# Kernel optimization log

Hardware: AMD Instinct MI355X
Metric: run time of the kernel (lower is better)

Reference implementation:

```python
import jax, jax.numpy as jnp
import numpy as np

N_NODES = 100000
N_EDGES = 3200000
N_GRAPHS = 512
IN_CH = 50
HID = 256


def setup_inputs() -> dict:
    key = jax.random.key(0)
    ks = jax.random.split(key, 8)
    x = jax.random.normal(ks[0], (N_NODES, IN_CH), dtype=jnp.float32)
    edge_index = jax.random.randint(ks[1], (2, N_EDGES), 0, N_NODES, dtype=jnp.int64)
    batch = jnp.sort(jax.random.randint(ks[2], (N_NODES,), 0, N_GRAPHS, dtype=jnp.int64))
    # SAGEConv params: lin_l (applied to aggregated neighbors, with bias), lin_r (root, no bias)
    s_in = 1.0 / np.sqrt(IN_CH)
    W_l = jax.random.uniform(ks[3], (HID, IN_CH), jnp.float32, -s_in, s_in)
    b_l = jax.random.uniform(ks[4], (HID,), jnp.float32, -s_in, s_in)
    W_r = jax.random.uniform(ks[5], (HID, IN_CH), jnp.float32, -s_in, s_in)
    s_h = 1.0 / np.sqrt(HID)
    W_c = jax.random.uniform(ks[6], (2, HID), jnp.float32, -s_h, s_h)
    b_c = jax.random.uniform(ks[7], (2,), jnp.float32, -s_h, s_h)
    return {"x": x, "edge_index": edge_index, "batch": batch,
            "W_l": W_l, "b_l": b_l, "W_r": W_r, "W_c": W_c, "b_c": b_c}


def _segment_mean(vals, seg_ids, num_segments):
    s = jax.ops.segment_sum(vals, seg_ids, num_segments=num_segments)
    cnt = jax.ops.segment_sum(jnp.ones((vals.shape[0],), vals.dtype), seg_ids,
                              num_segments=num_segments)
    return s / jnp.maximum(cnt, 1.0)[:, None]


def reference(x, edge_index, batch, W_l, b_l, W_r, W_c, b_c):
    src, dst = edge_index[0], edge_index[1]
    # SAGEConv: mean-aggregate neighbor features at each target node
    agg = _segment_mean(x[src], dst, N_NODES)          # [N, IN_CH]
    h = agg @ W_l.T + b_l + x @ W_r.T                  # [N, HID]
    h = jax.nn.leaky_relu(h, negative_slope=0.01)
    # dropout p=0.3 is identity in eval mode
    pooled = _segment_mean(h, batch, N_GRAPHS)         # [G, HID]
    return pooled @ W_c.T + b_c                        # [G, 2]
```

## Files before the change

### kernel.cpp

```cpp
#include <hip/hip_runtime.h>

#define N_NODES 100000
#define N_EDGES 3200000
#define N_GRAPHS 512
#define IN_CH 50
#define HID 256
#define NB 391
#define NBLK2 391
#define EPB2 8192

typedef unsigned short ushort_t;
using s16x8 = __attribute__((ext_vector_type(8))) short;
using us8   = __attribute__((ext_vector_type(8))) unsigned short;
using us4   = __attribute__((ext_vector_type(4))) unsigned short;
using f32x4 = __attribute__((ext_vector_type(4))) float;
using f32x2 = __attribute__((ext_vector_type(2))) float;

__device__ __forceinline__ float bf2f(ushort_t u) {
    return __uint_as_float(((unsigned int)u) << 16);
}
__device__ __forceinline__ ushort_t f2bf(float f) {
    unsigned int x = __float_as_uint(f);
    unsigned int r = x + 0x7fffu + ((x >> 16) & 1u);
    return (ushort_t)(r >> 16);
}
__device__ __forceinline__ int clampi(int v, int hi) {
    return v < 0 ? 0 : (v >= hi ? hi - 1 : v);
}

__device__ __forceinline__ unsigned char f2e4(float f) {
    unsigned char s = (unsigned char)((__float_as_uint(f) >> 31) << 7);
    float a = fabsf(f);
    if (a >= 0.015625f) {
        if (a > 448.f) a = 448.f;
        unsigned int u = __float_as_uint(a);
        u += 0x7FFFFu + ((u >> 20) & 1u);
        int e8 = (int)(u >> 23) - 127 + 7;
        unsigned int m8 = (u >> 20) & 7u;
        if (e8 > 15) { e8 = 15; m8 = 6; }
        return s | (unsigned char)((e8 << 3) | m8);
    } else {
        int m = (int)rintf(a * 512.f);
        if (m > 7) return s | 0x08;
        return s | (unsigned char)m;
    }
}
__device__ __forceinline__ float e42f(unsigned int c) {
    unsigned int w = ((c & 0x80u) << 24) | ((c & 0x7fu) << 20);
    return __uint_as_float(w) * 0x1p120f;
}

__device__ __forceinline__ void acc8(f32x2 a2[4], uint2 w, float m) {
#if __has_builtin(__builtin_amdgcn_cvt_pk_f32_fp8)
    f32x2 p0 = __builtin_amdgcn_cvt_pk_f32_fp8((int)w.x, false);
    f32x2 p1 = __builtin_amdgcn_cvt_pk_f32_fp8((int)w.x, true);
    f32x2 p2 = __builtin_amdgcn_cvt_pk_f32_fp8((int)w.y, false);
    f32x2 p3 = __builtin_amdgcn_cvt_pk_f32_fp8((int)w.y, true);
#else
    f32x2 p0, p1, p2, p3;
    p0[0] = e42f(w.x & 0xffu);         p0[1] = e42f((w.x >> 8) & 0xffu);
    p1[0] = e42f((w.x >> 16) & 0xffu); p1[1] = e42f((w.x >> 24) & 0xffu);
    p2[0] = e42f(w.y & 0xffu);         p2[1] = e42f((w.y >> 8) & 0xffu);
    p3[0] = e42f((w.y >> 16) & 0xffu); p3[1] = e42f((w.y >> 24) & 0xffu);
#endif
    a2[0] = p0 * m + a2[0];
    a2[1] = p1 * m + a2[1];
    a2[2] = p2 * m + a2[2];
    a2[3] = p3 * m + a2[3];
}

__device__ __forceinline__ void wavered(f32x2 a2[4]) {
#pragma unroll
    for (int p = 0; p < 4; ++p) {
        a2[p][0] += __shfl_xor(a2[p][0], 8);
        a2[p][1] += __shfl_xor(a2[p][1], 8);
        a2[p][0] += __shfl_xor(a2[p][0], 16);
        a2[p][1] += __shfl_xor(a2[p][1], 16);
        a2[p][0] += __shfl_xor(a2[p][0], 32);
        a2[p][1] += __shfl_xor(a2[p][1], 32);
    }
}

constexpr size_t OFF_GACC   = 0;
constexpr size_t ZBYTES     = 8192;
constexpr size_t OFF_AGG    = 561536;
constexpr size_t OFF_X8     = 13361536;
constexpr size_t OFF_EP     = 19761536;
constexpr size_t OFF_WT     = 32573824;
constexpr size_t OFF_BND    = 32639360;
constexpr size_t OFF_LST    = 32641416;

__global__ __launch_bounds__(512) void k_scatter(const int* __restrict__ ei,
                                                 int* __restrict__ ep,
                                                 ushort_t* __restrict__ lst) {
    __shared__ int hist[NB];
    __shared__ int sa[512];
    __shared__ int sorig[512];
    __shared__ int lstart[NB + 1];
    __shared__ int lcur[NB];
    __shared__ unsigned int eph[EPB2];

    const int blk = blockIdx.x, t = threadIdx.x;
    for (int i = t; i < NB; i += 512) hist[i] = 0;
    __syncthreads();
    const int e0 = blk * EPB2;
    int sv[16], dv[16];
#pragma unroll
    for (int j = 0; j < 16; ++j) {
        int e = e0 + j * 512 + t;
        if (e < N_EDGES) {
            sv[j] = clampi(ei[e], N_NODES);
            dv[j] = clampi(ei[N_EDGES + e], N_NODES);
        } else {
            dv[j] = -1;
        }
    }
#pragma unroll
    for (int j = 0; j < 16; ++j)
        if (dv[j] >= 0) atomicAdd(&hist[dv[j] >> 8], 1);
    __syncthreads();
    int v = (t < NB) ? hist[t] : 0;
    sa[t] = v; sorig[t] = v;
    __syncthreads();
    for (int off = 1; off < 512; off <<= 1) {
        int u = (t >= off) ? sa[t - off] : 0;
        __syncthreads();
        sa[t] += u;
        __syncthreads();
    }
    if (t < NB) { lstart[t] = sa[t] - sorig[t]; lcur[t] = sa[t] - sorig[t]; }
    if (t == NB - 1) lstart[NB] = sa[t];
    __syncthreads();
#pragma unroll
    for (int j = 0; j < 16; ++j) {
        if (dv[j] >= 0) {
            int b = dv[j] >> 8;
            int r = atomicAdd(&lcur[b], 1);
            eph[r] = ((unsigned int)sv[j] << 8) | (unsigned int)(dv[j] & 255);
        }
    }
    __syncthreads();
    int mv = lstart[NB];
    for (int i = t; i < mv; i += 512) ep[e0 + i] = (int)eph[i];
    for (int i = t; i <= NB; i += 512) lst[blk * (NB + 1) + i] = (ushort_t)lstart[i];
}

#define PREP_CONV_BLOCKS 6250
#define PREP_BW_BLOCKS 128
#define PREP_BND_BLOCKS 391
__global__ __launch_bounds__(256) void k_prep(const float* __restrict__ x,
                                              unsigned char* __restrict__ x8,
                                              const float* __restrict__ Wl,
                                              const float* __restrict__ Wr,
                                              ushort_t* __restrict__ WT,
                                              const int* __restrict__ batch,
                                              int* __restrict__ bnd) {
    int blk = blockIdx.x;
    if (blk < PREP_CONV_BLOCKS) {
        int idx = blk * 256 + threadIdx.x;
        int n = idx >> 4, c4 = (idx & 15) << 2;
        uchar4 o;
        o.x = (c4 + 0 < IN_CH) ? f2e4(x[n * IN_CH + c4 + 0]) : (unsigned char)0;
        o.y = (c4 + 1 < IN_CH) ? f2e4(x[n * IN_CH + c4 + 1]) : (unsigned char)0;
        o.z = (c4 + 2 < IN_CH) ? f2e4(x[n * IN_CH + c4 + 2]) : (unsigned char)0;
        o.w = (c4 + 3 < IN_CH) ? f2e4(x[n * IN_CH + c4 + 3]) : (unsigned char)0;
        *(uchar4*)(x8 + (size_t)n * 64 + c4) = o;
    } else if (blk < PREP_CONV_BLOCKS + PREP_BW_BLOCKS) {
        int idx = (blk - PREP_CONV_BLOCKS) * 256 + threadIdx.x;
        int j = idx >> 7;
        int k = idx & 127;
        ushort_t val = 0;
        if (k < IN_CH) val = f2bf(Wl[j * IN_CH + k]);
        else if (k >= 64 && k < 64 + IN_CH) val = f2bf(Wr[j * IN_CH + (k - 64)]);
        WT[idx] = val;
    } else {
        int n = (blk - PREP_CONV_BLOCKS - PREP_BW_BLOCKS) * 256 + threadIdx.x;
        if (n >= N_NODES) return;
        int b = clampi(batch[n], N_GRAPHS);
        if (n == 0) {
            for (int g = 0; g <= b; ++g) bnd[g] = 0;
        } else {
            int a = clampi(batch[n - 1], N_GRAPHS);
            for (int g = a + 1; g <= b; ++g) bnd[g] = n;
        }
        if (n == N_NODES - 1) {
            for (int g = b + 1; g <= N_GRAPHS; ++g) bnd[g] = N_NODES;
        }
    }
}

#define CSR_CAP 10240
__global__ __launch_bounds__(512) void k_csrgather(const int* __restrict__ ep,
                                                   const ushort_t* __restrict__ lst,
                                                   const unsigned char* __restrict__ x8,
                                                   ushort_t* __restrict__ agg) {
    __shared__ int sa[512];
    __shared__ int sorig[512];
    __shared__ int rro[NBLK2 + 1];
    __shared__ int lsa[NBLK2];
    __shared__ int ldeg[256];
    __shared__ int lcur[256];
    __shared__ int excl_s[256];
    __shared__ int lds_src[CSR_CAP];
    ushort_t* runof = (ushort_t*)lds_src;

    const int b = blockIdx.x, t = threadIdx.x;

    int lenv = 0;
    if (t < NBLK2) {
        int lsv = (int)lst[t * (NB + 1) + b];
        int le = (int)lst[t * (NB + 1) + b + 1];
        lenv = le - lsv;
        lsa[t] = lsv;
    }
    sa[t] = lenv; sorig[t] = lenv;
    __syncthreads();
    for (int off = 1; off < 512; off <<= 1) {
        int u = (t >= off) ? sa[t - off] : 0;
        __syncthreads();
        sa[t] += u;
        __syncthreads();
    }
    if (t < NBLK2) rro[t] = sa[t] - sorig[t];
    if (t == NBLK2 - 1) rro[NBLK2] = sa[t];
    __syncthreads();
    int m = rro[NBLK2];
    if (m > CSR_CAP) m = CSR_CAP;

    if (t < NBLK2) {
        int o = rro[t];
        int e = o + lenv;
        if (e > CSR_CAP) e = CSR_CAP;
        for (int j = o; j < e; ++j) runof[j] = (ushort_t)t;
    }
    if (t < 256) ldeg[t] = 0;
    __syncthreads();

    int rv[20];
#pragma unroll
    for (int k = 0; k < 20; ++k) {
        int i = t + k * 512;
        if (i < m) {
            int r = (int)runof[i];
            rv[k] = ep[r * EPB2 + lsa[r] + (i - rro[r])];
        }
    }
#pragma unroll
    for (int k = 0; k < 20; ++k) {
        int i = t + k * 512;
        if (i < m) atomicAdd(&ldeg[rv[k] & 255], 1);
    }
    __syncthreads();
    if (t < 256) sa[t] = ldeg[t];
    __syncthreads();
    for (int off = 1; off < 256; off <<= 1) {
        int u = (t >= off && t < 256) ? sa[t - off] : 0;
        __syncthreads();
        if (t < 256) sa[t] += u;
        __syncthreads();
    }
    if (t < 256) {
        int excl = sa[t] - ldeg[t];
        excl_s[t] = excl;
        lcur[t] = excl;
    }
    __syncthreads();
#pragma unroll
    for (int k = 0; k < 20; ++k) {
        int i = t + k * 512;
        if (i < m) {
            int p = rv[k];
            int r = atomicAdd(&lcur[p & 255], 1);
            lds_src[r] = p >> 8;
        }
    }
    __syncthreads();

    const int wv = t >> 6;
    const int lane = t & 63;
    const int r8 = lane >> 3;
    const int c8 = lane & 7;
    const int cb = c8 << 3;
    for (int k = 0; k < 32; k += 2) {
        int ln0 = wv * 32 + k;
        int gid0 = (b << 8) + ln0;
        if (gid0 >= N_NODES) break;
        int ok1 = (gid0 + 1 < N_NODES) ? 1 : 0;
        int dg0 = ldeg[ln0], st0 = excl_s[ln0];
        int dg1 = ok1 ? ldeg[ln0 + 1] : 0;
        int st1 = ok1 ? excl_s[ln0 + 1] : st0;

        f32x2 a2[4] = {};
        f32x2 c2[4] = {};
        int dgm = dg0 > dg1 ? dg0 : dg1;
        int nit = (dgm + 31) >> 5;
        for (int it = 0; it < nit; ++it) {
            int i0 = (it << 5) + r8;
            int i1 = i0 + 8, i2 = i0 + 16, i3 = i0 + 24;
            int sA = lds_src[st0 + (i0 < dg0 ? i0 : 0)];
            int sB = lds_src[st0 + (i1 < dg0 ? i1 : 0)];
            int sC = lds_src[st0 + (i2 < dg0 ? i2 : 0)];
            int sD = lds_src[st0 + (i3 < dg0 ? i3 : 0)];
            int sE = lds_src[st1 + (i0 < dg1 ? i0 : 0)];
            int sF = lds_src[st1 + (i1 < dg1 ? i1 : 0)];
            int sG = lds_src[st1 + (i2 < dg1 ? i2 : 0)];
            int sH = lds_src[st1 + (i3 < dg1 ? i3 : 0)];
            uint2 wA = *(const uint2*)(x8 + (size_t)sA * 64 + cb);
            uint2 wB = *(const uint2*)(x8 + (size_t)sB * 64 + cb);
            uint2 wC = *(const uint2*)(x8 + (size_t)sC * 64 + cb);
            uint2 wD = *(const uint2*)(x8 + (size_t)sD * 64 + cb);
            uint2 wE = *(const uint2*)(x8 + (size_t)sE * 64 + cb);
            uint2 wF = *(const uint2*)(x8 + (size_t)sF * 64 + cb);
            uint2 wG = *(const uint2*)(x8 + (size_t)sG * 64 + cb);
            uint2 wH = *(const uint2*)(x8 + (size_t)sH * 64 + cb);
            acc8(a2, wA, i0 < dg0 ? 1.f : 0.f);
            acc8(a2, wB, i1 < dg0 ? 1.f : 0.f);
            acc8(a2, wC, i2 < dg0 ? 1.f : 0.f);
            acc8(a2, wD, i3 < dg0 ? 1.f : 0.f);
            acc8(c2, wE, i0 < dg1 ? 1.f : 0.f);
            acc8(c2, wF, i1 < dg1 ? 1.f : 0.f);
            acc8(c2, wG, i2 < dg1 ? 1.f : 0.f);
            acc8(c2, wH, i3 < dg1 ? 1.f : 0.f);
        }
        wavered(a2);
        wavered(c2);
        if (r8 == 0) {
            float inv0 = 1.0f / (float)(dg0 > 1 ? dg0 : 1);
            us8 o;
#pragma unroll
            for (int q = 0; q < 8; ++q) o[q] = f2bf(a2[q >> 1][q & 1] * inv0);
            *(us8*)(agg + (size_t)gid0 * 64 + cb) = o;
            if (ok1) {
                float inv1 = 1.0f / (float)(dg1 > 1 ? dg1 : 1);
                us8 o1;
#pragma unroll
                for (int q = 0; q < 8; ++q) o1[q] = f2bf(c2[q >> 1][q & 1] * inv1);
                *(us8*)(agg + (size_t)(gid0 + 1) * 64 + cb) = o1;
            }
        }
    }
}

__global__ __launch_bounds__(256) void k_convb(const float* __restrict__ x,
                                               ushort_t* __restrict__ xb) {
    int t = blockIdx.x * blockDim.x + threadIdx.x;
    if (t >= N_NODES * 16) return;
    int n = t >> 4, c4 = (t & 15) << 2;
    us4 o;
#pragma unroll
    for (int j = 0; j < 4; j++) {
        int c = c4 + j;
        o[j] = (c < IN_CH) ? f2bf(x[n * IN_CH + c]) : (ushort_t)0;
    }
    *(us4*)(xb + (size_t)n * 64 + c4) = o;
}

__global__ __launch_bounds__(256) void k_gemm(const ushort_t* __restrict__ agg,
                                              const ushort_t* __restrict__ xb,
                                              const ushort_t* __restrict__ WT,
                                              const float* __restrict__ bl,
                                              const float* __restrict__ Wc,
                                              const int* __restrict__ batch,
                                              float* __restrict__ gacc) {
    __shared__ ushort_t Alds[64 * 136];
    __shared__ f32x2 yp[4][64][17];
    __shared__ float gred[64][2];

    const int t = threadIdx.x;
    const int w = t >> 6;
    const int lane = t & 63;
    const int quad = lane >> 4;
    const int r16 = lane & 15;
    const int brow0 = blockIdx.x * 128;

    if (t < 128) gred[t >> 1][t & 1] = 0.f;

    s16x8 bfr[4][4];
#pragma unroll
    for (int s = 0; s < 4; ++s)
#pragma unroll
        for (int ni = 0; ni < 4; ++ni)
            bfr[s][ni] = *(const s16x8*)(WT + (size_t)(w * 64 + 16 * ni + r16) * 128
                                            + s * 32 + (quad << 3));

    float blv[4], w0v[4], w1v[4];
#pragma unroll
    for (int ni = 0; ni < 4; ni++) {
        int col = w * 64 + 16 * ni + r16;
        blv[ni] = bl[col];
        w0v[ni] = Wc[col];
        w1v[ni] = Wc[HID + col];
    }

    int lastb = brow0 + 127;
    if (lastb >= N_NODES) lastb = N_NODES - 1;
    const int gmin = clampi(batch[brow0], N_GRAPHS);
    const int gmax = clampi(batch[lastb], N_GRAPHS);
    const int gspan = gmax - gmin + 1;
    const bool use_lds = (gspan <= 64);

    for (int r4 = 0; r4 < 2; ++r4) {
        const int row0 = brow0 + r4 * 64;
        __syncthreads();
        {
            int row = t >> 2;
            int q4 = t & 3;
            int gr = row0 + row;
            us8* dst = (us8*)&Alds[row * 136 + q4 * 32];
            if (gr < N_NODES) {
                const us8* src = (q4 < 2)
                    ? (const us8*)(agg + (size_t)gr * 64 + (q4 & 1) * 32)
                    : (const us8*)(xb + (size_t)gr * 64 + (q4 & 1) * 32);
                dst[0] = src[0];
                dst[1] = src[1];
                dst[2] = src[2];
                dst[3] = src[3];
            } else {
                us8 z = {0, 0, 0, 0, 0, 0, 0, 0};
                dst[0] = z; dst[1] = z; dst[2] = z; dst[3] = z;
            }
        }
        __syncthreads();

        f32x4 acc[4][4] = {};
#pragma unroll
        for (int s = 0; s < 4; ++s) {
            s16x8 af[4];
#pragma unroll
            for (int mi = 0; mi < 4; mi++)
                af[mi] = *(const s16x8*)&Alds[(16 * mi + r16) * 136 + s * 32 + (quad << 3)];
#pragma unroll
            for (int mi = 0; mi < 4; mi++)
#pragma unroll
                for (int ni = 0; ni < 4; ni++)
                    acc[mi][ni] = __builtin_amdgcn_mfma_f32_16x16x32_bf16(
                        af[mi], bfr[s][ni], acc[mi][ni], 0, 0, 0);
        }

#pragma unroll
        for (int mi = 0; mi < 4; mi++) {
#pragma unroll
            for (int r = 0; r < 4; r++) {
                float p0 = 0.f, p1 = 0.f;
#pragma unroll
                for (int ni = 0; ni < 4; ni++) {
                    float h = acc[mi][ni][r] + blv[ni];
                    h = (h > 0.f) ? h : 0.01f * h;
                    p0 = fmaf(h, w0v[ni], p0);
                    p1 = fmaf(h, w1v[ni], p1);
                }
                int rl = 16 * mi + (quad << 2) + r;
                f32x2 pv; pv[0] = p0; pv[1] = p1;
                yp[w][rl][r16] = pv;
            }
        }
        __syncthreads();

        if (t < 64) {
            f32x2 s; s[0] = 0.f; s[1] = 0.f;
#pragma unroll
            for (int ww = 0; ww < 4; ++ww)
#pragma unroll
                for (int j = 0; j < 16; ++j)
                    s = s + yp[ww][t][j];
            int node = row0 + t;
            if (node < N_NODES) {
                int g = clampi(batch[node], N_GRAPHS);
                if (use_lds) {
                    atomicAdd(&gred[g - gmin][0], s[0]);
                    atomicAdd(&gred[g - gmin][1], s[1]);
                } else {
                    atomicAdd(&gacc[g * 2 + 0], s[0]);
                    atomicAdd(&gacc[g * 2 + 1], s[1]);
                }
            }
        }
    }
    __syncthreads();
    if (use_lds && t < gspan * 2) {
        int gg = t >> 1, c2 = t & 1;
        float v = gred[gg][c2];
        if (v != 0.f) atomicAdd(&gacc[(gmin + gg) * 2 + c2], v);
    }
}

__global__ void k_fin(const float* __restrict__ gacc, const int* __restrict__ bnd,
                      const float* __restrict__ bc, float* __restrict__ out) {
    int t = blockIdx.x * blockDim.x + threadIdx.x;
    if (t < N_GRAPHS * 2) {
        int g = t >> 1, c = t & 1;
        int cnt = bnd[g + 1] - bnd[g];
        out[t] = gacc[t] / (float)(cnt > 1 ? cnt : 1) + bc[c];
    }
}

extern "C" void kernel_launch(void* const* d_in, const int* in_sizes, int n_in,
                              void* d_out, int out_size, void* d_ws, size_t ws_size,
                              hipStream_t stream) {
    const float* x  = (const float*)d_in[0];
    const int* ei   = (const int*)d_in[1];
    const int* batch= (const int*)d_in[2];
    const float* Wl = (const float*)d_in[3];
    const float* bl = (const float*)d_in[4];
    const float* Wr = (const float*)d_in[5];
    const float* Wc = (const float*)d_in[6];
    const float* bc = (const float*)d_in[7];
    float* out = (float*)d_out;

    char* ws = (char*)d_ws;
    float* gacc        = (float*)(ws + OFF_GACC);
    ushort_t* agg      = (ushort_t*)(ws + OFF_AGG);
    unsigned char* x8  = (unsigned char*)(ws + OFF_X8);
    int* ep            = (int*)(ws + OFF_EP);
    ushort_t* xb       = (ushort_t*)(ws + OFF_EP);
    ushort_t* WT       = (ushort_t*)(ws + OFF_WT);
    int* bnd           = (int*)(ws + OFF_BND);
    ushort_t* lst      = (ushort_t*)(ws + OFF_LST);

    hipMemsetAsync(ws, 0, ZBYTES, stream);
    k_scatter    <<<NBLK2, 512, 0, stream>>>(ei, ep, lst);
    k_prep       <<<PREP_CONV_BLOCKS + PREP_BW_BLOCKS + PREP_BND_BLOCKS, 256, 0, stream>>>(
                     x, x8, Wl, Wr, WT, batch, bnd);
    k_csrgather  <<<NB, 512, 0, stream>>>(ep, lst, x8, agg);
    k_convb      <<<(N_NODES * 16 + 255) / 256, 256, 0, stream>>>(x, xb);
    k_gemm       <<<(N_NODES + 127) / 128, 256, 0, stream>>>(agg, xb, WT, bl, Wc, batch, gacc);
    k_fin        <<<4, 256, 0, stream>>>(gacc, bnd, bc, out);
}
```

Baseline: 209.3 us.

## Fuse scatter and prep kernels; gather four nodes per wave iteration

```diff
diff --git a/kernel.cpp b/kernel.cpp
--- a/kernel.cpp
+++ b/kernel.cpp
@@ -90,9 +90,20 @@
 constexpr size_t OFF_BND    = 32639360;
 constexpr size_t OFF_LST    = 32641416;
 
-__global__ __launch_bounds__(512) void k_scatter(const int* __restrict__ ei,
-                                                 int* __restrict__ ep,
-                                                 ushort_t* __restrict__ lst) {
+#define SP_SCAT 391
+#define SP_CONV 3125
+#define SP_BW   64
+#define SP_BND  196
+__global__ __launch_bounds__(512) void k_sp(const int* __restrict__ ei,
+                                            int* __restrict__ ep,
+                                            ushort_t* __restrict__ lst,
+                                            const float* __restrict__ x,
+                                            unsigned char* __restrict__ x8,
+                                            const float* __restrict__ Wl,
+                                            const float* __restrict__ Wr,
+                                            ushort_t* __restrict__ WT,
+                                            const int* __restrict__ batch,
+                                            int* __restrict__ bnd) {
     __shared__ int hist[NB];
     __shared__ int sa[512];
     __shared__ int sorig[512];
@@ -101,63 +112,51 @@
     __shared__ unsigned int eph[EPB2];
 
     const int blk = blockIdx.x, t = threadIdx.x;
-    for (int i = t; i < NB; i += 512) hist[i] = 0;
-    __syncthreads();
-    const int e0 = blk * EPB2;
-    int sv[16], dv[16];
-#pragma unroll
-    for (int j = 0; j < 16; ++j) {
-        int e = e0 + j * 512 + t;
-        if (e < N_EDGES) {
-            sv[j] = clampi(ei[e], N_NODES);
-            dv[j] = clampi(ei[N_EDGES + e], N_NODES);
-        } else {
-            dv[j] = -1;
-        }
-    }
-#pragma unroll
-    for (int j = 0; j < 16; ++j)
-        if (dv[j] >= 0) atomicAdd(&hist[dv[j] >> 8], 1);
-    __syncthreads();
-    int v = (t < NB) ? hist[t] : 0;
-    sa[t] = v; sorig[t] = v;
-    __syncthreads();
-    for (int off = 1; off < 512; off <<= 1) {
-        int u = (t >= off) ? sa[t - off] : 0;
-        __syncthreads();
-        sa[t] += u;
-        __syncthreads();
-    }
-    if (t < NB) { lstart[t] = sa[t] - sorig[t]; lcur[t] = sa[t] - sorig[t]; }
-    if (t == NB - 1) lstart[NB] = sa[t];
-    __syncthreads();
-#pragma unroll
-    for (int j = 0; j < 16; ++j) {
-        if (dv[j] >= 0) {
-            int b = dv[j] >> 8;
-            int r = atomicAdd(&lcur[b], 1);
-            eph[r] = ((unsigned int)sv[j] << 8) | (unsigned int)(dv[j] & 255);
-        }
-    }
-    __syncthreads();
-    int mv = lstart[NB];
-    for (int i = t; i < mv; i += 512) ep[e0 + i] = (int)eph[i];
-    for (int i = t; i <= NB; i += 512) lst[blk * (NB + 1) + i] = (ushort_t)lstart[i];
-}
-
-#define PREP_CONV_BLOCKS 6250
-#define PREP_BW_BLOCKS 128
-#define PREP_BND_BLOCKS 391
-__global__ __launch_bounds__(256) void k_prep(const float* __restrict__ x,
-                                              unsigned char* __restrict__ x8,
-                                              const float* __restrict__ Wl,
-                                              const float* __restrict__ Wr,
-                                              ushort_t* __restrict__ WT,
-                                              const int* __restrict__ batch,
-                                              int* __restrict__ bnd) {
-    int blk = blockIdx.x;
-    if (blk < PREP_CONV_BLOCKS) {
-        int idx = blk * 256 + threadIdx.x;
+    if (blk < SP_SCAT) {
+        for (int i = t; i < NB; i += 512) hist[i] = 0;
+        __syncthreads();
+        const int e0 = blk * EPB2;
+        int sv[16], dv[16];
+#pragma unroll
+        for (int j = 0; j < 16; ++j) {
+            int e = e0 + j * 512 + t;
+            if (e < N_EDGES) {
+                sv[j] = clampi(ei[e], N_NODES);
+                dv[j] = clampi(ei[N_EDGES + e], N_NODES);
+            } else {
+                dv[j] = -1;
+            }
+        }
+#pragma unroll
+        for (int j = 0; j < 16; ++j)
+            if (dv[j] >= 0) atomicAdd(&hist[dv[j] >> 8], 1);
+        __syncthreads();
+        int v = (t < NB) ? hist[t] : 0;
+        sa[t] = v; sorig[t] = v;
+        __syncthreads();
+        for (int off = 1; off < 512; off <<= 1) {
+            int u = (t >= off) ? sa[t - off] : 0;
+            __syncthreads();
+            sa[t] += u;
+            __syncthreads();
+        }
+        if (t < NB) { lstart[t] = sa[t] - sorig[t]; lcur[t] = sa[t] - sorig[t]; }
+        if (t == NB - 1) lstart[NB] = sa[t];
+        __syncthreads();
+#pragma unroll
+        for (int j = 0; j < 16; ++j) {
+            if (dv[j] >= 0) {
+                int b = dv[j] >> 8;
+                int r = atomicAdd(&lcur[b], 1);
+                eph[r] = ((unsigned int)sv[j] << 8) | (unsigned int)(dv[j] & 255);
+            }
+        }
+        __syncthreads();
+        int mv = lstart[NB];
+        for (int i = t; i < mv; i += 512) ep[e0 + i] = (int)eph[i];
+        for (int i = t; i <= NB; i += 512) lst[blk * (NB + 1) + i] = (ushort_t)lstart[i];
+    } else if (blk < SP_SCAT + SP_CONV) {
+        int idx = (blk - SP_SCAT) * 512 + t;
         int n = idx >> 4, c4 = (idx & 15) << 2;
         uchar4 o;
         o.x = (c4 + 0 < IN_CH) ? f2e4(x[n * IN_CH + c4 + 0]) : (unsigned char)0;
@@ -165,8 +164,8 @@
         o.z = (c4 + 2 < IN_CH) ? f2e4(x[n * IN_CH + c4 + 2]) : (unsigned char)0;
         o.w = (c4 + 3 < IN_CH) ? f2e4(x[n * IN_CH + c4 + 3]) : (unsigned char)0;
         *(uchar4*)(x8 + (size_t)n * 64 + c4) = o;
-    } else if (blk < PREP_CONV_BLOCKS + PREP_BW_BLOCKS) {
-        int idx = (blk - PREP_CONV_BLOCKS) * 256 + threadIdx.x;
+    } else if (blk < SP_SCAT + SP_CONV + SP_BW) {
+        int idx = (blk - SP_SCAT - SP_CONV) * 512 + t;
         int j = idx >> 7;
         int k = idx & 127;
         ushort_t val = 0;
@@ -174,7 +173,7 @@
         else if (k >= 64 && k < 64 + IN_CH) val = f2bf(Wr[j * IN_CH + (k - 64)]);
         WT[idx] = val;
     } else {
-        int n = (blk - PREP_CONV_BLOCKS - PREP_BW_BLOCKS) * 256 + threadIdx.x;
+        int n = (blk - SP_SCAT - SP_CONV - SP_BW) * 512 + t;
         if (n >= N_NODES) return;
         int b = clampi(batch[n], N_GRAPHS);
         if (n == 0) {
@@ -281,61 +280,60 @@
     const int r8 = lane >> 3;
     const int c8 = lane & 7;
     const int cb = c8 << 3;
-    for (int k = 0; k < 32; k += 2) {
-        int ln0 = wv * 32 + k;
-        int gid0 = (b << 8) + ln0;
-        if (gid0 >= N_NODES) break;
-        int ok1 = (gid0 + 1 < N_NODES) ? 1 : 0;
-        int dg0 = ldeg[ln0], st0 = excl_s[ln0];
-        int dg1 = ok1 ? ldeg[ln0 + 1] : 0;
-        int st1 = ok1 ? excl_s[ln0 + 1] : st0;
-
-        f32x2 a2[4] = {};
-        f32x2 c2[4] = {};
-        int dgm = dg0 > dg1 ? dg0 : dg1;
+    for (int k = 0; k < 32; k += 4) {
+        int ln = wv * 32 + k;
+        int gid = (b << 8) + ln;
+        if (gid >= N_NODES) break;
+        int dg[4], st[4];
+#pragma unroll
+        for (int j = 0; j < 4; ++j) {
+            bool ok = (gid + j) < N_NODES;
+            dg[j] = ok ? ldeg[ln + j] : 0;
+            st[j] = ok ? excl_s[ln + j] : excl_s[ln];
+        }
+        f32x2 ac[4][4];
+#pragma unroll
+        for (int j = 0; j < 4; ++j)
+#pragma unroll
+            for (int p = 0; p < 4; ++p) { ac[j][p][0] = 0.f; ac[j][p][1] = 0.f; }
+        int dgm = dg[0];
+#pragma unroll
+        for (int j = 1; j < 4; ++j) dgm = dg[j] > dgm ? dg[j] : dgm;
         int nit = (dgm + 31) >> 5;
         for (int it = 0; it < nit; ++it) {
-            int i0 = (it << 5) + r8;
-            int i1 = i0 + 8, i2 = i0 + 16, i3 = i0 + 24;
-            int sA = lds_src[st0 + (i0 < dg0 ? i0 : 0)];
-            int sB = lds_src[st0 + (i1 < dg0 ? i1 : 0)];
-            int sC = lds_src[st0 + (i2 < dg0 ? i2 : 0)];
-            int sD = lds_src[st0 + (i3 < dg0 ? i3 : 0)];
-            int sE = lds_src[st1 + (i0 < dg1 ? i0 : 0)];
-            int sF = lds_src[st1 + (i1 < dg1 ? i1 : 0)];
-            int sG = lds_src[st1 + (i2 < dg1 ? i2 : 0)];
-            int sH = lds_src[st1 + (i3 < dg1 ? i3 : 0)];
-            uint2 wA = *(const uint2*)(x8 + (size_t)sA * 64 + cb);
-            uint2 wB = *(const uint2*)(x8 + (size_t)sB * 64 + cb);
-            uint2 wC = *(const uint2*)(x8 + (size_t)sC * 64 + cb);
-            uint2 wD = *(const uint2*)(x8 + (size_t)sD * 64 + cb);
-            uint2 wE = *(const uint2*)(x8 + (size_t)sE * 64 + cb);
-            uint2 wF = *(const uint2*)(x8 + (size_t)sF * 64 + cb);
-            uint2 wG = *(const uint2*)(x8 + (size_t)sG * 64 + cb);
-            uint2 wH = *(const uint2*)(x8 + (size_t)sH * 64 + cb);
-            acc8(a2, wA, i0 < dg0 ? 1.f : 0.f);
-            acc8(a2, wB, i1 < dg0 ? 1.f : 0.f);
-            acc8(a2, wC, i2 < dg0 ? 1.f : 0.f);
-            acc8(a2, wD, i3 < dg0 ? 1.f : 0.f);
-            acc8(c2, wE, i0 < dg1 ? 1.f : 0.f);
-            acc8(c2, wF, i1 < dg1 ? 1.f : 0.f);
-            acc8(c2, wG, i2 < dg1 ? 1.f : 0.f);
-            acc8(c2, wH, i3 < dg1 ? 1.f : 0.f);
-        }
-        wavered(a2);
-        wavered(c2);
+            int bi = (it << 5) + r8;
+            int idx[4][4];
+#pragma unroll
+            for (int j = 0; j < 4; ++j)
+#pragma unroll
+                for (int q = 0; q < 4; ++q) {
+                    int i = bi + q * 8;
+                    idx[j][q] = lds_src[st[j] + (i < dg[j] ? i : 0)];
+                }
+            uint2 wd[4][4];
+#pragma unroll
+            for (int j = 0; j < 4; ++j)
+#pragma unroll
+                for (int q = 0; q < 4; ++q)
+                    wd[j][q] = *(const uint2*)(x8 + (size_t)idx[j][q] * 64 + cb);
+#pragma unroll
+            for (int j = 0; j < 4; ++j)
+#pragma unroll
+                for (int q = 0; q < 4; ++q)
+                    acc8(ac[j], wd[j][q], (bi + q * 8) < dg[j] ? 1.f : 0.f);
+        }
+#pragma unroll
+        for (int j = 0; j < 4; ++j) wavered(ac[j]);
         if (r8 == 0) {
-            float inv0 = 1.0f / (float)(dg0 > 1 ? dg0 : 1);
-            us8 o;
-#pragma unroll
-            for (int q = 0; q < 8; ++q) o[q] = f2bf(a2[q >> 1][q & 1] * inv0);
-            *(us8*)(agg + (size_t)gid0 * 64 + cb) = o;
-            if (ok1) {
-                float inv1 = 1.0f / (float)(dg1 > 1 ? dg1 : 1);
-                us8 o1;
-#pragma unroll
-                for (int q = 0; q < 8; ++q) o1[q] = f2bf(c2[q >> 1][q & 1] * inv1);
-                *(us8*)(agg + (size_t)(gid0 + 1) * 64 + cb) = o1;
+#pragma unroll
+            for (int j = 0; j < 4; ++j) {
+                if (gid + j < N_NODES) {
+                    float inv = 1.0f / (float)(dg[j] > 1 ? dg[j] : 1);
+                    us8 o;
+#pragma unroll
+                    for (int q = 0; q < 8; ++q) o[q] = f2bf(ac[j][q >> 1][q & 1] * inv);
+                    *(us8*)(agg + (size_t)(gid + j) * 64 + cb) = o;
+                }
             }
         }
     }
@@ -518,9 +516,8 @@
     ushort_t* lst      = (ushort_t*)(ws + OFF_LST);
 
     hipMemsetAsync(ws, 0, ZBYTES, stream);
-    k_scatter    <<<NBLK2, 512, 0, stream>>>(ei, ep, lst);
-    k_prep       <<<PREP_CONV_BLOCKS + PREP_BW_BLOCKS + PREP_BND_BLOCKS, 256, 0, stream>>>(
-                     x, x8, Wl, Wr, WT, batch, bnd);
+    k_sp         <<<SP_SCAT + SP_CONV + SP_BW + SP_BND, 512, 0, stream>>>(
+                     ei, ep, lst, x, x8, Wl, Wr, WT, batch, bnd);
     k_csrgather  <<<NB, 512, 0, stream>>>(ep, lst, x8, agg);
     k_convb      <<<(N_NODES * 16 + 255) / 256, 256, 0, stream>>>(x, xb);
     k_gemm       <<<(N_NODES + 127) / 128, 256, 0, stream>>>(agg, xb, WT, bl, Wc, batch, gacc);
```

Result: slower. 223.1 us (+6.6%).
